# Optimization experiments

Hardware: AMD Instinct MI355X
Metric: run time of the kernel (lower is better)

## Reference

```python
import jax, jax.numpy as jnp
import numpy as np

D_MODEL = 1024
HEAD = 16
D_K = D_MODEL // HEAD


def setup_inputs() -> dict:
    key = jax.random.key(0)
    ks = jax.random.split(key, 6)
    B, S = 2, 2048
    scale = 1.0 / np.sqrt(D_MODEL)
    return {
        "q": jax.random.normal(ks[0], (B, S, D_MODEL), dtype=jnp.float32),
        "k": jax.random.normal(ks[1], (B, S, D_MODEL), dtype=jnp.float32),
        "v": jax.random.normal(ks[2], (B, S, D_MODEL), dtype=jnp.float32),
        "W_q": jax.random.normal(ks[3], (D_MODEL, D_MODEL), dtype=jnp.float32) * scale,
        "W_k": jax.random.normal(ks[4], (D_MODEL, D_MODEL), dtype=jnp.float32) * scale,
        "W_v": jax.random.normal(ks[5], (D_MODEL, D_MODEL), dtype=jnp.float32) * scale,
    }


def reference(q, k, v, W_q, W_k, W_v):
    B, S, _ = q.shape
    # nn.Linear: y = x @ W.T ; then split heads (B,S,H,dk) -> (B,H,S,dk) -> (B*H,S,dk)
    def proj(x, W):
        y = jnp.einsum('bsd,ed->bse', x, W)
        return y.reshape(B, S, HEAD, D_K).transpose(0, 2, 1, 3).reshape(B * HEAD, S, D_K)

    qh = proj(q, W_q)
    kh = proj(k, W_k)
    vh = proj(v, W_v)

    scores = jnp.einsum('nsd,ntd->nst', qh, kh) / np.sqrt(D_K).astype(np.float32)
    attn = jax.nn.softmax(scores, axis=2)
    out = jnp.einsum('nst,ntd->nsd', attn, vh)  # (B*H, S, dk), flat index = b*H + h

    # Faithful torch.chunk(dim=0, head) + torch.cat(dim=2):
    # chunk c = rows [c*B:(c+1)*B]; concatenated along feature dim.
    out = out.reshape(HEAD, B, S, D_K).transpose(1, 2, 0, 3).reshape(B, S, D_MODEL)
    return out
```

## Files before the change

### kernel.cpp

```cpp
#include <hip/hip_runtime.h>
#include <hip/hip_bf16.h>
#include <stdint.h>

typedef unsigned short u16;
typedef __attribute__((ext_vector_type(8))) short bf16x8;
typedef __attribute__((ext_vector_type(8))) _Float16 f16x8;
typedef __attribute__((ext_vector_type(4))) float f32x4;
typedef __attribute__((ext_vector_type(4))) u16 u16x4;
typedef __attribute__((ext_vector_type(4))) float f4v;

#define DEV __device__ __forceinline__

DEV u16 f2bf(float x) {
    union { float f; uint32_t u; } v; v.f = x;
    uint32_t r = v.u + 0x7FFF + ((v.u >> 16) & 1);
    return (u16)(r >> 16);
}

DEV float fexp2(float x) {
    float r;
    asm("v_exp_f32 %0, %1" : "=v"(r) : "v"(x));
    return r;
}

DEV f32x4 mfma16(bf16x8 a, bf16x8 b, f32x4 c) {
    return __builtin_amdgcn_mfma_f32_16x16x32_bf16(a, b, c, 0, 0, 0);
}
DEV f32x4 mfma16h(f16x8 a, f16x8 b, f32x4 c) {
    return __builtin_amdgcn_mfma_f32_16x16x32_f16(a, b, c, 0, 0, 0);
}

DEV void gld_lds16(const u16* g, u16* lds) {
    __builtin_amdgcn_global_load_lds(
        (const __attribute__((address_space(1))) void*)g,
        (__attribute__((address_space(3))) void*)lds, 16, 0, 0);
}

#define VMCNT2 asm volatile("s_waitcnt vmcnt(2)" ::: "memory")
#define VMCNT0 asm volatile("s_waitcnt vmcnt(0)" ::: "memory")
#define BAR() __builtin_amdgcn_s_barrier()

DEV u16 h2u(_Float16 h) { union { _Float16 h; u16 u; } v; v.h = h; return v.u; }

struct PrepArgs {
    const float* src[6];
    u16* dst[6];
    int n4[6];
};

__global__ __launch_bounds__(256) void prep_kernel(PrepArgs a) {
    const int z = blockIdx.y;
    const f4v* __restrict__ src = (const f4v*)a.src[z];
    u16x4* __restrict__ dst = (u16x4*)a.dst[z];
    const int n4 = a.n4[z];
    int i = blockIdx.x * blockDim.x + threadIdx.x;
    const int stride = gridDim.x * blockDim.x;
    for (; i < n4; i += stride) {
        f4v x = src[i];
        u16x4 d;
#pragma unroll
        for (int c = 0; c < 4; ++c) d[c] = h2u((_Float16)x[c]);
        dst[i] = d;
    }
}

struct ProjArgs {
    const u16* xf[3];
    const u16* wf[3];
    u16* outq;
    u16* outk;
    u16* outvt;
};

__global__ __launch_bounds__(512, 2) void proj_kernel(ProjArgs args) {
    __shared__ u16 lds[2][32768];

    const int tid = threadIdx.x;
    const int w = tid >> 6, l = tid & 63;
    const int fr = l & 15, fg = l >> 4;
    const int wa = w >> 2, wb = w & 3;

    const int b0 = blockIdx.x;
    const int swz = (b0 & 7) * 24 + (b0 >> 3);
    const int z = swz >> 6;
    const int r = swz & 63;

    int ta, tb;
    const u16 *A0, *B0;
    if (z < 2) {
        ta = r & 3; tb = r >> 2;
        A0 = args.wf[z];
        B0 = args.xf[z];
    } else {
        ta = r >> 2; tb = r & 3;
        A0 = args.xf[2];
        B0 = args.wf[2];
    }

    const int s_r = tid >> 3;
    const int s_c = (((tid & 7) ^ (s_r & 7)) << 3);
    const size_t aoff = (size_t)(ta * 256 + s_r) * 1024 + s_c;
    const size_t boff = (size_t)(tb * 256 + s_r) * 1024 + s_c;

    const int abase = (wa * 128 + fr) * 64;
    const int bbase = 16384 + (wb * 64 + fr) * 64;
    const int sl0 = ((fg) ^ (fr & 7)) << 3;
    const int sl1 = ((4 + fg) ^ (fr & 7)) << 3;

    f32x4 acc[8][4];
#pragma unroll
    for (int mi = 0; mi < 8; ++mi)
#pragma unroll
        for (int ni = 0; ni < 4; ++ni)
            acc[mi][ni] = (f32x4){0.f, 0.f, 0.f, 0.f};

#define STAGE2(SRC, OFFBASE, REGION, HALF, BUFN, KTN)                               \
    do {                                                                            \
        _Pragma("unroll")                                                           \
        for (int j = 0; j < 2; ++j) {                                               \
            gld_lds16((SRC) + (OFFBASE) + (size_t)((HALF) * 128 + j * 64) * 1024    \
                           + (size_t)(KTN) * 64,                                    \
                      &lds[BUFN][(REGION) + (HALF) * 8192 + j * 4096 + w * 512]);   \
        }                                                                           \
    } while (0)

#pragma unroll
    for (int h = 0; h < 2; ++h) {
#pragma unroll
        for (int j = 0; j < 2; ++j) {
            gld_lds16(A0 + aoff + (size_t)(h * 128 + j * 64) * 1024,
                      &lds[0][h * 8192 + j * 4096 + w * 512]);
            gld_lds16(B0 + boff + (size_t)(h * 128 + j * 64) * 1024,
                      &lds[0][16384 + h * 8192 + j * 4096 + w * 512]);
        }
    }

#define PHASE(MQ0, STAGECALL)                                                       \
    do {                                                                            \
        if (more) STAGECALL;                                                        \
        f16x8 p00 = *(const f16x8*)&Lb[abase + (MQ0) * 1024 + sl0];                 \
        f16x8 p01 = *(const f16x8*)&Lb[abase + (MQ0) * 1024 + sl1];                 \
        f16x8 p10 = *(const f16x8*)&Lb[abase + (MQ0 + 1) * 1024 + sl0];             \
        f16x8 p11 = *(const f16x8*)&Lb[abase + (MQ0 + 1) * 1024 + sl1];             \
        BAR();                                                                      \
        __builtin_amdgcn_s_setprio(1);                                              \
        _Pragma("unroll")                                                           \
        for (int ni = 0; ni < 4; ++ni) {                                            \
            acc[MQ0][ni] = mfma16h(p00, Bf0[ni], acc[MQ0][ni]);                     \
            acc[MQ0][ni] = mfma16h(p01, Bf1[ni], acc[MQ0][ni]);                     \
            acc[MQ0 + 1][ni] = mfma16h(p10, Bf0[ni], acc[MQ0 + 1][ni]);             \
            acc[MQ0 + 1][ni] = mfma16h(p11, Bf1[ni], acc[MQ0 + 1][ni]);             \
        }                                                                           \
        __builtin_amdgcn_s_setprio(0);                                              \
        BAR();                                                                      \
    } while (0)

#pragma unroll 1
    for (int t = 0; t < 16; ++t) {
        const int buf = t & 1;
        const int nbuf = buf ^ 1;
        const int tn = t + 1;
        const bool more = (tn < 16);
        const int ktn = tn;
        const u16* An = A0;
        const u16* Bn = B0;
        const u16* Lb = &lds[buf][0];

        f16x8 Bf0[4], Bf1[4];

        if (more) STAGE2(An, aoff, 0, 0, nbuf, ktn);
        if (more) { VMCNT2; } else { VMCNT0; }
        BAR();
        {
            f16x8 a00 = *(const f16x8*)&Lb[abase + sl0];
            f16x8 a01 = *(const f16x8*)&Lb[abase + sl1];
            f16x8 a10 = *(const f16x8*)&Lb[abase + 1024 + sl0];
            f16x8 a11 = *(const f16x8*)&Lb[abase + 1024 + sl1];
#pragma unroll
            for (int ni = 0; ni < 4; ++ni) {
                Bf0[ni] = *(const f16x8*)&Lb[bbase + ni * 1024 + sl0];
                Bf1[ni] = *(const f16x8*)&Lb[bbase + ni * 1024 + sl1];
            }
            BAR();
            __builtin_amdgcn_s_setprio(1);
#pragma unroll
            for (int ni = 0; ni < 4; ++ni) {
                acc[0][ni] = mfma16h(a00, Bf0[ni], acc[0][ni]);
                acc[0][ni] = mfma16h(a01, Bf1[ni], acc[0][ni]);
                acc[1][ni] = mfma16h(a10, Bf0[ni], acc[1][ni]);
                acc[1][ni] = mfma16h(a11, Bf1[ni], acc[1][ni]);
            }
            __builtin_amdgcn_s_setprio(0);
            BAR();
        }
        PHASE(2, STAGE2(An, aoff, 0, 1, nbuf, ktn));
        PHASE(4, STAGE2(Bn, boff, 16384, 0, nbuf, ktn));
        PHASE(6, STAGE2(Bn, boff, 16384, 1, nbuf, ktn));
    }
#undef PHASE
#undef STAGE2

    if (z < 2) {
        u16* outp = (z == 0) ? args.outq : args.outk;
#pragma unroll
        for (int mq = 0; mq < 8; ++mq) {
#pragma unroll
            for (int ni = 0; ni < 4; ++ni) {
                const int e0 = ta * 256 + wa * 128 + mq * 16 + fg * 4;
                const int m = tb * 256 + wb * 64 + ni * 16 + fr;
                const int n = (m >> 11) * 16 + (e0 >> 6);
                const int s = m & 2047;
                u16x4 pk;
#pragma unroll
                for (int rr = 0; rr < 4; ++rr) pk[rr] = f2bf(acc[mq][ni][rr]);
                *(u16x4*)&outp[((size_t)(n * 2048 + s)) * 64 + (e0 & 63)] = pk;
            }
        }
    } else {
        u16* outp = args.outvt;
#pragma unroll
        for (int mq = 0; mq < 8; ++mq) {
#pragma unroll
            for (int ni = 0; ni < 4; ++ni) {
                const int m0 = ta * 256 + wa * 128 + mq * 16 + fg * 4;
                const int e = tb * 256 + wb * 64 + ni * 16 + fr;
                const int n = (m0 >> 11) * 16 + (e >> 6);
                u16x4 pk;
#pragma unroll
                for (int rr = 0; rr < 4; ++rr) pk[rr] = f2bf(acc[mq][ni][rr]);
                *(u16x4*)&outp[((size_t)(n * 64 + (e & 63))) * 2048 + (m0 & 2047)] = pk;
            }
        }
    }
}

__global__ __launch_bounds__(512, 4) void attn_kernel(const u16* __restrict__ qh,
                                                      const u16* __restrict__ kh,
                                                      const u16* __restrict__ vt,
                                                      float* __restrict__ out) {
    __shared__ u16 lds[2][16384];

    const int tid = threadIdx.x;
    const int w = tid >> 6, l = tid & 63;
    const int fr = l & 15, fg = l >> 4;

    const int b = blockIdx.x;
    const int n = (b & 7) * 4 + ((b >> 3) >> 4);
    const int qt = (b >> 3) & 15;
    const int qbase = qt * 128 + w * 16;
    const float cs = 0.125f * 1.44269504088896f;

    const u16* khn = kh + (size_t)n * 2048 * 64;
    const u16* vtn = vt + (size_t)n * 64 * 2048;

    const u16* qrow = qh + ((size_t)n * 2048 + qbase + fr) * 64;
    bf16x8 aq0 = *(const bf16x8*)(qrow + fg * 8);
    bf16x8 aq1 = *(const bf16x8*)(qrow + 32 + fg * 8);

    bf16x8 ones;
#pragma unroll
    for (int j = 0; j < 8; ++j) ones[j] = (short)0x3F80;

    const int krow_s = tid >> 2;
    const int kcol_s = (tid & 3) * 16;
    const int kg_s = ((tid >> 2) & 3) + 4 * ((tid >> 5) & 1);
    const int kws0 = ((((tid & 3) * 2 + 0) + kg_s) & 7) * 8;
    const int kws1 = ((((tid & 3) * 2 + 1) + kg_s) & 7) * 8;
    const int vrow_s = tid >> 3;
    const int vcol_s = (tid & 7) * 16;
    const int vg_s = (tid >> 3) & 7;
    const int vws0 = ((((tid & 7) * 2 + 0) + vg_s) & 15) * 8;
    const int vws1 = ((((tid & 7) * 2 + 1) + vg_s) & 15) * 8;

    const int rbase = ((fr >> 2) << 3) + (fr & 3);
    const int kg_r = (fr & 3) + 4 * ((fr >> 2) & 1);
    const int ksl0 = (((fg + 0) + kg_r) & 7) * 8;
    const int ksl1 = (((fg + 4) + kg_r) & 7) * 8;
    const int vg_r = fr & 7;

    f32x4 acc[5];
#pragma unroll
    for (int dc = 0; dc < 5; ++dc) acc[dc] = (f32x4){0.f, 0.f, 0.f, 0.f};
    float mrun = -INFINITY;

    bf16x8 kr0, kr1, vr0, vr1;

#define STAGE_LOAD(kb_) do {                                                       \
        const u16* ksrc = khn + ((size_t)((kb_) * 128 + krow_s)) * 64 + kcol_s;    \
        kr0 = *(const bf16x8*)(ksrc);                                              \
        kr1 = *(const bf16x8*)(ksrc + 8);                                          \
        const u16* vsrc = vtn + (size_t)vrow_s * 2048 + (kb_) * 128 + vcol_s;      \
        vr0 = *(const bf16x8*)(vsrc);                                              \
        vr1 = *(const bf16x8*)(vsrc + 8);                                          \
    } while (0)

#define STAGE_WRITE(buf_) do {                                                     \
        u16* kp = &lds[buf_][0];                                                   \
        *(bf16x8*)&kp[krow_s * 64 + kws0] = kr0;                                   \
        *(bf16x8*)&kp[krow_s * 64 + kws1] = kr1;                                   \
        u16* vp = &lds[buf_][8192];                                                \
        *(bf16x8*)&vp[vrow_s * 128 + vws0] = vr0;                                  \
        *(bf16x8*)&vp[vrow_s * 128 + vws1] = vr1;                                  \
    } while (0)

    STAGE_LOAD(0);
    STAGE_WRITE(0);
    STAGE_LOAD(1);
    __syncthreads();

    for (int kb = 0; kb < 16; ++kb) {
        const int cur = kb & 1;
        const u16* Kb = &lds[cur][0];
        const u16* Vb = &lds[cur][8192];

        f32x4 sf[8];
        __builtin_amdgcn_s_setprio(1);
#pragma unroll
        for (int c = 0; c < 8; ++c) {
            const int rr = ((c >> 1) << 5) + ((c & 1) << 2) + rbase;
            f32x4 s = (f32x4){0.f, 0.f, 0.f, 0.f};
            s = mfma16(*(const bf16x8*)&Kb[rr * 64 + ksl0], aq0, s);
            s = mfma16(*(const bf16x8*)&Kb[rr * 64 + ksl1], aq1, s);
            sf[c] = s;
        }
        __builtin_amdgcn_s_setprio(0);

        f32x4 cmv = sf[0];
#pragma unroll
        for (int c = 1; c < 8; ++c)
#pragma unroll
            for (int rr = 0; rr < 4; ++rr) cmv[rr] = fmaxf(cmv[rr], sf[c][rr]);
        float cm = fmaxf(fmaxf(cmv[0], cmv[1]), fmaxf(cmv[2], cmv[3]));
        cm = fmaxf(cm, __shfl_xor(cm, 16, 64));
        cm = fmaxf(cm, __shfl_xor(cm, 32, 64));

        if (__any(cm > mrun)) {
            float mnew = fmaxf(mrun, cm);
            float sc = fexp2(cs * (mrun - mnew));
            mrun = mnew;
#pragma unroll
            for (int dc = 0; dc < 5; ++dc)
#pragma unroll
                for (int rr = 0; rr < 4; ++rr) acc[dc][rr] *= sc;
        }

        const float negm = -cs * mrun;
#pragma unroll
        for (int c = 0; c < 8; ++c) {
#pragma unroll
            for (int rr = 0; rr < 4; ++rr)
                sf[c][rr] = fexp2(fmaf(cs, sf[c][rr], negm));
        }

        if (kb < 15) {
            STAGE_WRITE(cur ^ 1);
            if (kb < 14) STAGE_LOAD(kb + 2);
        }

        __builtin_amdgcn_s_setprio(1);
#pragma unroll
        for (int pw = 0; pw < 4; ++pw) {
            union { bf16x8 v; uint32_t u[4]; } ap;
#pragma unroll
            for (int q2 = 0; q2 < 4; ++q2) {
                float lo = sf[2 * pw + (q2 >> 1)][(q2 & 1) * 2 + 0];
                float hi = sf[2 * pw + (q2 >> 1)][(q2 & 1) * 2 + 1];
                asm("v_cvt_pk_bf16_f32 %0, %1, %2" : "=v"(ap.u[q2]) : "v"(lo), "v"(hi));
            }
#pragma unroll
            for (int dc = 0; dc < 4; ++dc) {
                const int vsl = (((pw * 4 + fg) + vg_r) & 15) * 8;
                acc[dc] = mfma16(*(const bf16x8*)&Vb[(dc * 16 + fr) * 128 + vsl],
                                 ap.v, acc[dc]);
            }
            acc[4] = mfma16(ones, ap.v, acc[4]);
        }
        __builtin_amdgcn_s_setprio(0);

        if (kb < 15) __syncthreads();
    }

    const float inv = 1.f / acc[4][0];
    const int bq = n & 1;
    const int col0 = (n >> 1) * 64;
    float* orow = out + ((size_t)bq * 2048 + qbase + fr) * 1024 + col0 + fg * 4;
#pragma unroll
    for (int dblk = 0; dblk < 4; ++dblk) {
        f4v o;
#pragma unroll
        for (int rr = 0; rr < 4; ++rr) o[rr] = acc[dblk][rr] * inv;
        *(f4v*)&orow[dblk * 16] = o;
    }
#undef STAGE_LOAD
#undef STAGE_WRITE
}

extern "C" void kernel_launch(void* const* d_in, const int* in_sizes, int n_in,
                              void* d_out, int out_size, void* d_ws, size_t ws_size,
                              hipStream_t stream) {
    (void)n_in; (void)out_size; (void)ws_size;
    const float* q  = (const float*)d_in[0];
    const float* k  = (const float*)d_in[1];
    const float* v  = (const float*)d_in[2];
    const float* Wq = (const float*)d_in[3];
    const float* Wk = (const float*)d_in[4];
    const float* Wv = (const float*)d_in[5];

    uint8_t* ws = (uint8_t*)d_ws;
    const size_t MB = 1024ull * 1024ull;
    u16* xq_f = (u16*)(ws + 0 * MB);
    u16* xk_f = (u16*)(ws + 8 * MB);
    u16* xv_f = (u16*)(ws + 16 * MB);
    u16* wq_f = (u16*)(ws + 24 * MB);
    u16* wk_f = (u16*)(ws + 26 * MB);
    u16* wv_f = (u16*)(ws + 28 * MB);
    u16* qh   = (u16*)(ws + 30 * MB);
    u16* kh   = (u16*)(ws + 38 * MB);
    u16* vt   = (u16*)(ws + 46 * MB);

    PrepArgs pp;
    pp.src[0] = q;  pp.src[1] = k;  pp.src[2] = v;
    pp.src[3] = Wq; pp.src[4] = Wk; pp.src[5] = Wv;
    pp.dst[0] = xq_f; pp.dst[1] = xk_f; pp.dst[2] = xv_f;
    pp.dst[3] = wq_f; pp.dst[4] = wk_f; pp.dst[5] = wv_f;
    pp.n4[0] = pp.n4[1] = pp.n4[2] = in_sizes[0] / 4;
    pp.n4[3] = pp.n4[4] = pp.n4[5] = in_sizes[3] / 4;
    prep_kernel<<<dim3(1024, 6), 256, 0, stream>>>(pp);

    ProjArgs pa;
    pa.xf[0] = xq_f; pa.xf[1] = xk_f; pa.xf[2] = xv_f;
    pa.wf[0] = wq_f; pa.wf[1] = wk_f; pa.wf[2] = wv_f;
    pa.outq = qh; pa.outk = kh; pa.outvt = vt;
    proj_kernel<<<dim3(192), 512, 0, stream>>>(pa);

    attn_kernel<<<dim3(512), 512, 0, stream>>>(qh, kh, vt, (float*)d_out);
}
```

Measured before the change: 102.4 us.

## Split KV range across two warp groups with 32-row Q tiles per wave

The attention kernel now splits the 8 waves into two groups that each process half of the key/value sequence in 64-key chunks. Each wave handles 32 query rows (two 16-row tiles), so every K and V fragment read from LDS feeds two MFMAs. The row sum is now computed with VALU adds instead of an extra MFMA against a ones vector. The two partial softmax states are merged through LDS at the end, which adds a final reduction phase, an extra barrier and more accumulator registers.

After: 112.2 us. 9.6% more time.

```diff
diff --git a/kernel.cpp b/kernel.cpp
--- a/kernel.cpp
+++ b/kernel.cpp
@@ -238,69 +238,77 @@
                                                       const u16* __restrict__ kh,
                                                       const u16* __restrict__ vt,
                                                       float* __restrict__ out) {
-    __shared__ u16 lds[2][16384];
+    __shared__ u16 lds[2][2][8192];
 
     const int tid = threadIdx.x;
     const int w = tid >> 6, l = tid & 63;
     const int fr = l & 15, fg = l >> 4;
+    const int g = w >> 2, wq = w & 3;
 
     const int b = blockIdx.x;
     const int n = (b & 7) * 4 + ((b >> 3) >> 4);
     const int qt = (b >> 3) & 15;
-    const int qbase = qt * 128 + w * 16;
+    const int qbase = qt * 128 + wq * 32;
     const float cs = 0.125f * 1.44269504088896f;
 
-    const u16* khn = kh + (size_t)n * 2048 * 64;
-    const u16* vtn = vt + (size_t)n * 64 * 2048;
-
-    const u16* qrow = qh + ((size_t)n * 2048 + qbase + fr) * 64;
-    bf16x8 aq0 = *(const bf16x8*)(qrow + fg * 8);
-    bf16x8 aq1 = *(const bf16x8*)(qrow + 32 + fg * 8);
-
-    bf16x8 ones;
-#pragma unroll
-    for (int j = 0; j < 8; ++j) ones[j] = (short)0x3F80;
-
-    const int krow_s = tid >> 2;
-    const int kcol_s = (tid & 3) * 16;
-    const int kg_s = ((tid >> 2) & 3) + 4 * ((tid >> 5) & 1);
-    const int kws0 = ((((tid & 3) * 2 + 0) + kg_s) & 7) * 8;
-    const int kws1 = ((((tid & 3) * 2 + 1) + kg_s) & 7) * 8;
-    const int vrow_s = tid >> 3;
-    const int vcol_s = (tid & 7) * 16;
-    const int vg_s = (tid >> 3) & 7;
-    const int vws0 = ((((tid & 7) * 2 + 0) + vg_s) & 15) * 8;
-    const int vws1 = ((((tid & 7) * 2 + 1) + vg_s) & 15) * 8;
+    const u16* khn = kh + ((size_t)n * 2048 + g * 1024) * 64;
+    const u16* vtn = vt + (size_t)n * 64 * 2048 + g * 1024;
+
+    bf16x8 aqA0, aqA1, aqB0, aqB1;
+    {
+        const u16* qrA = qh + ((size_t)n * 2048 + qbase + fr) * 64;
+        aqA0 = *(const bf16x8*)(qrA + fg * 8);
+        aqA1 = *(const bf16x8*)(qrA + 32 + fg * 8);
+        const u16* qrB = qrA + 16 * 64;
+        aqB0 = *(const bf16x8*)(qrB + fg * 8);
+        aqB1 = *(const bf16x8*)(qrB + 32 + fg * 8);
+    }
+
+    const int st = tid & 255;
+    const int srow = st >> 2;
+    const int sj = st & 3;
+    const int kg_s = (srow & 3) + 4 * ((srow >> 3) & 1);
+    const int kws0 = (((sj * 2 + 0) + kg_s) & 7) * 8;
+    const int kws1 = (((sj * 2 + 1) + kg_s) & 7) * 8;
+    const int vg_s = srow & 7;
+    const int vws0 = (((sj * 2 + 0) + vg_s) & 7) * 8;
+    const int vws1 = (((sj * 2 + 1) + vg_s) & 7) * 8;
 
     const int rbase = ((fr >> 2) << 3) + (fr & 3);
     const int kg_r = (fr & 3) + 4 * ((fr >> 2) & 1);
-    const int ksl0 = (((fg + 0) + kg_r) & 7) * 8;
-    const int ksl1 = (((fg + 4) + kg_r) & 7) * 8;
+    const int ksl0 = ((fg + kg_r) & 7) * 8;
+    const int ksl1 = ((fg + 4 + kg_r) & 7) * 8;
     const int vg_r = fr & 7;
-
-    f32x4 acc[5];
-#pragma unroll
-    for (int dc = 0; dc < 5; ++dc) acc[dc] = (f32x4){0.f, 0.f, 0.f, 0.f};
-    float mrun = -INFINITY;
+    const int vsl0 = ((fg + vg_r) & 7) * 8;
+    const int vsl1 = ((4 + fg + vg_r) & 7) * 8;
+
+    f32x4 accA[4], accB[4];
+#pragma unroll
+    for (int dc = 0; dc < 4; ++dc) {
+        accA[dc] = (f32x4){0.f, 0.f, 0.f, 0.f};
+        accB[dc] = (f32x4){0.f, 0.f, 0.f, 0.f};
+    }
+    float mA = -INFINITY, mB = -INFINITY;
+    float lA = 0.f, lB = 0.f;
 
     bf16x8 kr0, kr1, vr0, vr1;
 
-#define STAGE_LOAD(kb_) do {                                                       \
-        const u16* ksrc = khn + ((size_t)((kb_) * 128 + krow_s)) * 64 + kcol_s;    \
-        kr0 = *(const bf16x8*)(ksrc);                                              \
-        kr1 = *(const bf16x8*)(ksrc + 8);                                          \
-        const u16* vsrc = vtn + (size_t)vrow_s * 2048 + (kb_) * 128 + vcol_s;      \
-        vr0 = *(const bf16x8*)(vsrc);                                              \
-        vr1 = *(const bf16x8*)(vsrc + 8);                                          \
+#define STAGE_LOAD(c_) do {                                                         \
+        const u16* ksrc = khn + ((size_t)((c_) * 64 + srow)) * 64 + sj * 16;        \
+        kr0 = *(const bf16x8*)(ksrc);                                               \
+        kr1 = *(const bf16x8*)(ksrc + 8);                                           \
+        const u16* vsrc = vtn + (size_t)srow * 2048 + (c_) * 64 + sj * 16;          \
+        vr0 = *(const bf16x8*)(vsrc);                                               \
+        vr1 = *(const bf16x8*)(vsrc + 8);                                           \
     } while (0)
 
-#define STAGE_WRITE(buf_) do {                                                     \
-        u16* kp = &lds[buf_][0];                                                   \
-        *(bf16x8*)&kp[krow_s * 64 + kws0] = kr0;                                   \
-        *(bf16x8*)&kp[krow_s * 64 + kws1] = kr1;                                   \
-        u16* vp = &lds[buf_][8192];                                                \
-        *(bf16x8*)&vp[vrow_s * 128 + vws0] = vr0;                                  \
-        *(bf16x8*)&vp[vrow_s * 128 + vws1] = vr1;                                  \
+#define STAGE_WRITE(buf_) do {                                                      \
+        u16* kp = &lds[buf_][g][0];                                                 \
+        *(bf16x8*)&kp[srow * 64 + kws0] = kr0;                                      \
+        *(bf16x8*)&kp[srow * 64 + kws1] = kr1;                                      \
+        u16* vp = &lds[buf_][g][4096];                                              \
+        *(bf16x8*)&vp[srow * 64 + vws0] = vr0;                                      \
+        *(bf16x8*)&vp[srow * 64 + vws1] = vr1;                                      \
     } while (0)
 
     STAGE_LOAD(0);
@@ -308,88 +316,177 @@
     STAGE_LOAD(1);
     __syncthreads();
 
-    for (int kb = 0; kb < 16; ++kb) {
-        const int cur = kb & 1;
-        const u16* Kb = &lds[cur][0];
-        const u16* Vb = &lds[cur][8192];
-
-        f32x4 sf[8];
+    for (int c = 0; c < 16; ++c) {
+        const int cur = c & 1;
+        const u16* Kb = &lds[cur][g][0];
+        const u16* Vb = &lds[cur][g][4096];
+
+        f32x4 sA[4], sB[4];
         __builtin_amdgcn_s_setprio(1);
 #pragma unroll
-        for (int c = 0; c < 8; ++c) {
-            const int rr = ((c >> 1) << 5) + ((c & 1) << 2) + rbase;
-            f32x4 s = (f32x4){0.f, 0.f, 0.f, 0.f};
-            s = mfma16(*(const bf16x8*)&Kb[rr * 64 + ksl0], aq0, s);
-            s = mfma16(*(const bf16x8*)&Kb[rr * 64 + ksl1], aq1, s);
-            sf[c] = s;
+        for (int cc = 0; cc < 4; ++cc) {
+            const int rr = ((cc >> 1) << 5) + ((cc & 1) << 2) + rbase;
+            bf16x8 k0 = *(const bf16x8*)&Kb[rr * 64 + ksl0];
+            bf16x8 k1 = *(const bf16x8*)&Kb[rr * 64 + ksl1];
+            f32x4 z = (f32x4){0.f, 0.f, 0.f, 0.f};
+            sA[cc] = mfma16(k1, aqA1, mfma16(k0, aqA0, z));
+            sB[cc] = mfma16(k1, aqB1, mfma16(k0, aqB0, z));
         }
         __builtin_amdgcn_s_setprio(0);
 
-        f32x4 cmv = sf[0];
-#pragma unroll
-        for (int c = 1; c < 8; ++c)
-#pragma unroll
-            for (int rr = 0; rr < 4; ++rr) cmv[rr] = fmaxf(cmv[rr], sf[c][rr]);
-        float cm = fmaxf(fmaxf(cmv[0], cmv[1]), fmaxf(cmv[2], cmv[3]));
-        cm = fmaxf(cm, __shfl_xor(cm, 16, 64));
-        cm = fmaxf(cm, __shfl_xor(cm, 32, 64));
-
-        if (__any(cm > mrun)) {
-            float mnew = fmaxf(mrun, cm);
-            float sc = fexp2(cs * (mrun - mnew));
-            mrun = mnew;
-#pragma unroll
-            for (int dc = 0; dc < 5; ++dc)
-#pragma unroll
-                for (int rr = 0; rr < 4; ++rr) acc[dc][rr] *= sc;
-        }
-
-        const float negm = -cs * mrun;
-#pragma unroll
-        for (int c = 0; c < 8; ++c) {
-#pragma unroll
-            for (int rr = 0; rr < 4; ++rr)
-                sf[c][rr] = fexp2(fmaf(cs, sf[c][rr], negm));
-        }
-
-        if (kb < 15) {
+        bf16x8 apA[2], apB[2];
+
+        {
+            f32x4 cm4 = sA[0];
+#pragma unroll
+            for (int cc = 1; cc < 4; ++cc)
+#pragma unroll
+                for (int rr = 0; rr < 4; ++rr) cm4[rr] = fmaxf(cm4[rr], sA[cc][rr]);
+            float cm = fmaxf(fmaxf(cm4[0], cm4[1]), fmaxf(cm4[2], cm4[3]));
+            cm = fmaxf(cm, __shfl_xor(cm, 16, 64));
+            cm = fmaxf(cm, __shfl_xor(cm, 32, 64));
+            if (__any(cm > mA)) {
+                float mn = fmaxf(mA, cm);
+                float sc = fexp2(cs * (mA - mn));
+                mA = mn;
+                lA *= sc;
+#pragma unroll
+                for (int dc = 0; dc < 4; ++dc)
+#pragma unroll
+                    for (int rr = 0; rr < 4; ++rr) accA[dc][rr] *= sc;
+            }
+            const float negm = -cs * mA;
+            f32x4 ps = (f32x4){0.f, 0.f, 0.f, 0.f};
+#pragma unroll
+            for (int cc = 0; cc < 4; ++cc) {
+#pragma unroll
+                for (int rr = 0; rr < 4; ++rr)
+                    sA[cc][rr] = fexp2(fmaf(cs, sA[cc][rr], negm));
+                ps += sA[cc];
+            }
+            lA += (ps[0] + ps[1]) + (ps[2] + ps[3]);
+#pragma unroll
+            for (int pw = 0; pw < 2; ++pw) {
+                union { bf16x8 v; uint32_t u[4]; } t;
+#pragma unroll
+                for (int q2 = 0; q2 < 4; ++q2) {
+                    float lo = sA[2 * pw + (q2 >> 1)][(q2 & 1) * 2 + 0];
+                    float hi = sA[2 * pw + (q2 >> 1)][(q2 & 1) * 2 + 1];
+                    asm("v_cvt_pk_bf16_f32 %0, %1, %2" : "=v"(t.u[q2]) : "v"(lo), "v"(hi));
+                }
+                apA[pw] = t.v;
+            }
+        }
+        {
+            f32x4 cm4 = sB[0];
+#pragma unroll
+            for (int cc = 1; cc < 4; ++cc)
+#pragma unroll
+                for (int rr = 0; rr < 4; ++rr) cm4[rr] = fmaxf(cm4[rr], sB[cc][rr]);
+            float cm = fmaxf(fmaxf(cm4[0], cm4[1]), fmaxf(cm4[2], cm4[3]));
+            cm = fmaxf(cm, __shfl_xor(cm, 16, 64));
+            cm = fmaxf(cm, __shfl_xor(cm, 32, 64));
+            if (__any(cm > mB)) {
+                float mn = fmaxf(mB, cm);
+                float sc = fexp2(cs * (mB - mn));
+                mB = mn;
+                lB *= sc;
+#pragma unroll
+                for (int dc = 0; dc < 4; ++dc)
+#pragma unroll
+                    for (int rr = 0; rr < 4; ++rr) accB[dc][rr] *= sc;
+            }
+            const float negm = -cs * mB;
+            f32x4 ps = (f32x4){0.f, 0.f, 0.f, 0.f};
+#pragma unroll
+            for (int cc = 0; cc < 4; ++cc) {
+#pragma unroll
+                for (int rr = 0; rr < 4; ++rr)
+                    sB[cc][rr] = fexp2(fmaf(cs, sB[cc][rr], negm));
+                ps += sB[cc];
+            }
+            lB += (ps[0] + ps[1]) + (ps[2] + ps[3]);
+#pragma unroll
+            for (int pw = 0; pw < 2; ++pw) {
+                union { bf16x8 v; uint32_t u[4]; } t;
+#pragma unroll
+                for (int q2 = 0; q2 < 4; ++q2) {
+                    float lo = sB[2 * pw + (q2 >> 1)][(q2 & 1) * 2 + 0];
+                    float hi = sB[2 * pw + (q2 >> 1)][(q2 & 1) * 2 + 1];
+                    asm("v_cvt_pk_bf16_f32 %0, %1, %2" : "=v"(t.u[q2]) : "v"(lo), "v"(hi));
+                }
+                apB[pw] = t.v;
+            }
+        }
+
+        if (c < 15) {
             STAGE_WRITE(cur ^ 1);
-            if (kb < 14) STAGE_LOAD(kb + 2);
+            if (c < 14) STAGE_LOAD(c + 2);
         }
 
         __builtin_amdgcn_s_setprio(1);
 #pragma unroll
-        for (int pw = 0; pw < 4; ++pw) {
-            union { bf16x8 v; uint32_t u[4]; } ap;
-#pragma unroll
-            for (int q2 = 0; q2 < 4; ++q2) {
-                float lo = sf[2 * pw + (q2 >> 1)][(q2 & 1) * 2 + 0];
-                float hi = sf[2 * pw + (q2 >> 1)][(q2 & 1) * 2 + 1];
-                asm("v_cvt_pk_bf16_f32 %0, %1, %2" : "=v"(ap.u[q2]) : "v"(lo), "v"(hi));
-            }
+        for (int dc = 0; dc < 4; ++dc) {
+            bf16x8 v0 = *(const bf16x8*)&Vb[(dc * 16 + fr) * 64 + vsl0];
+            accA[dc] = mfma16(v0, apA[0], accA[dc]);
+            accB[dc] = mfma16(v0, apB[0], accB[dc]);
+            bf16x8 v1 = *(const bf16x8*)&Vb[(dc * 16 + fr) * 64 + vsl1];
+            accA[dc] = mfma16(v1, apA[1], accA[dc]);
+            accB[dc] = mfma16(v1, apB[1], accB[dc]);
+        }
+        __builtin_amdgcn_s_setprio(0);
+
+        if (c < 15) __syncthreads();
+    }
+
+    lA += __shfl_xor(lA, 16, 64);
+    lA += __shfl_xor(lA, 32, 64);
+    lB += __shfl_xor(lB, 16, 64);
+    lB += __shfl_xor(lB, 32, 64);
+
+    __syncthreads();
+    float* lf = (float*)&lds[0][0][0];
+    if (g == 1) {
+#pragma unroll
+        for (int s = 0; s < 2; ++s) {
 #pragma unroll
             for (int dc = 0; dc < 4; ++dc) {
-                const int vsl = (((pw * 4 + fg) + vg_r) & 15) * 8;
-                acc[dc] = mfma16(*(const bf16x8*)&Vb[(dc * 16 + fr) * 128 + vsl],
-                                 ap.v, acc[dc]);
-            }
-            acc[4] = mfma16(ones, ap.v, acc[4]);
-        }
-        __builtin_amdgcn_s_setprio(0);
-
-        if (kb < 15) __syncthreads();
-    }
-
-    const float inv = 1.f / acc[4][0];
-    const int bq = n & 1;
-    const int col0 = (n >> 1) * 64;
-    float* orow = out + ((size_t)bq * 2048 + qbase + fr) * 1024 + col0 + fg * 4;
-#pragma unroll
-    for (int dblk = 0; dblk < 4; ++dblk) {
-        f4v o;
-#pragma unroll
-        for (int rr = 0; rr < 4; ++rr) o[rr] = acc[dblk][rr] * inv;
-        *(f4v*)&orow[dblk * 16] = o;
+                const int sl = ((dc * 4 + fg + fr) & 15) * 4;
+                *(f4v*)&lf[(wq * 2 + s) * 1024 + fr * 64 + sl] = s ? accB[dc] : accA[dc];
+            }
+        }
+        if (fg == 0) {
+            lf[8192 + (wq * 32 + fr) * 2] = mA;
+            lf[8192 + (wq * 32 + fr) * 2 + 1] = lA;
+            lf[8192 + (wq * 32 + 16 + fr) * 2] = mB;
+            lf[8192 + (wq * 32 + 16 + fr) * 2 + 1] = lB;
+        }
+    }
+    __syncthreads();
+    if (g == 0) {
+#pragma unroll
+        for (int s = 0; s < 2; ++s) {
+            const float Bm = lf[8192 + (wq * 32 + s * 16 + fr) * 2];
+            const float Bl = lf[8192 + (wq * 32 + s * 16 + fr) * 2 + 1];
+            const float ml = s ? mB : mA;
+            const float ll = s ? lB : lA;
+            const float mf = fmaxf(ml, Bm);
+            const float a0 = fexp2(cs * (ml - mf));
+            const float a1 = fexp2(cs * (Bm - mf));
+            const float inv = 1.f / (ll * a0 + Bl * a1);
+            float* orow = out + ((size_t)(n & 1) * 2048 + qbase + s * 16 + fr) * 1024
+                          + (n >> 1) * 64 + fg * 4;
+#pragma unroll
+            for (int dc = 0; dc < 4; ++dc) {
+                const int sl = ((dc * 4 + fg + fr) & 15) * 4;
+                f4v bv = *(const f4v*)&lf[(wq * 2 + s) * 1024 + fr * 64 + sl];
+                f4v av = s ? accB[dc] : accA[dc];
+                f4v o;
+#pragma unroll
+                for (int rr = 0; rr < 4; ++rr) o[rr] = (av[rr] * a0 + bv[rr] * a1) * inv;
+                *(f4v*)&orow[dc * 16] = o;
+            }
+        }
     }
 #undef STAGE_LOAD
 #undef STAGE_WRITE
```
